# Performance work log

Measured on AMD Instinct MI355X. Metric: run time of the kernel, lower is better.

The kernel has to match this reference:

```python
import jax, jax.numpy as jnp
import numpy as np

N = 50000
NEG_SLOPE = 0.2  # PyG GATConv default negative_slope


def gat_conv(x, src, dst, W, a_src, a_dst, bias, concat):
    """One PyG-style GATConv (eval mode, self-loops already in src/dst).
    x: [N, F_in], W: [F_in, H*C], a_src/a_dst: [H, C], bias: [H*C] or [C].
    """
    H, C = a_src.shape
    xl = (x @ W).reshape(N, H, C)                      # [N, H, C]
    alpha_src = jnp.sum(xl * a_src, axis=-1)           # [N, H]
    alpha_dst = jnp.sum(xl * a_dst, axis=-1)           # [N, H]
    e = jax.nn.leaky_relu(alpha_src[src] + alpha_dst[dst], NEG_SLOPE)  # [E, H]
    # edge-softmax over incoming edges of each destination node
    m = jax.ops.segment_max(e, dst, num_segments=N)    # [N, H]
    e = jnp.exp(e - m[dst])
    s = jax.ops.segment_sum(e, dst, num_segments=N)    # [N, H]
    alpha = e / s[dst]                                 # [E, H]
    msg = xl[src] * alpha[:, :, None]                  # [E, H, C]
    out = jax.ops.segment_sum(msg, dst, num_segments=N)  # [N, H, C]
    out = out.reshape(N, H * C) if concat else out.mean(axis=1)
    return out + bias


def setup_inputs() -> dict:
    key = jax.random.key(0)
    ks = jax.random.split(key, 10)
    in_ch, hid, out_ch, heads = 128, 64, 64, 4
    E = 800000
    x = jax.random.normal(ks[0], (N, in_ch), dtype=jnp.float32)
    edge_index = jax.random.randint(ks[1], (2, E), 0, N, dtype=jnp.int64)
    s1 = 1.0 / np.sqrt(in_ch)
    s2 = 1.0 / np.sqrt(hid * heads)
    return {
        "x": x,
        "edge_index": edge_index,
        "W1": jax.random.normal(ks[2], (in_ch, heads * hid), jnp.float32) * s1,
        "att_src1": jax.random.normal(ks[3], (heads, hid), jnp.float32) * s1,
        "att_dst1": jax.random.normal(ks[4], (heads, hid), jnp.float32) * s1,
        "b1": jnp.zeros((heads * hid,), jnp.float32),
        "W2": jax.random.normal(ks[5], (heads * hid, out_ch), jnp.float32) * s2,
        "att_src2": jax.random.normal(ks[6], (1, out_ch), jnp.float32) * s2,
        "att_dst2": jax.random.normal(ks[7], (1, out_ch), jnp.float32) * s2,
        "b2": jnp.zeros((out_ch,), jnp.float32),
    }


def reference(x, edge_index, W1, att_src1, att_dst1, b1, W2, att_src2, att_dst2, b2):
    # PyG GATConv adds self-loops by default
    loops = jnp.arange(N, dtype=edge_index.dtype)
    src = jnp.concatenate([edge_index[0], loops])
    dst = jnp.concatenate([edge_index[1], loops])
    h = gat_conv(x, src, dst, W1, att_src1, att_dst1, b1, concat=True)
    h = jax.nn.elu(h)  # dropout is identity in eval mode
    out = gat_conv(h, src, dst, W2, att_src2, att_dst2, b2, concat=False)
    return out
```

## Files before the change

### kernel.cpp

```cpp
#include <hip/hip_runtime.h>
#include <math.h>


typedef unsigned short u16;
typedef short s8v __attribute__((ext_vector_type(8)));
typedef float f32x4 __attribute__((ext_vector_type(4)));

#define LOG2E 1.4426950408889634f

__device__ __forceinline__ float bflo(unsigned int u) {
  return __builtin_bit_cast(float, u << 16);
}
__device__ __forceinline__ float bfhi(unsigned int u) {
  return __builtin_bit_cast(float, u & 0xffff0000u);
}
__device__ __forceinline__ u16 f2bf(float f) {
  unsigned int u = __builtin_bit_cast(unsigned int, f);
  return (u16)((u + 0x7fff + ((u >> 16) & 1)) >> 16);
}


__global__ void prep_count_kernel(const int* __restrict__ ei, int E, int Nn,
                                  int* __restrict__ deg,
                                  const float* __restrict__ W1, u16* __restrict__ W1T,
                                  const float* __restrict__ W2, u16* __restrict__ W2T) {
  int i = blockIdx.x * blockDim.x + threadIdx.x;
  int Et = E + Nn;
  if (i < Et) {
    int dst = (i < E) ? ei[E + i] : (i - E);
    atomicAdd(&deg[dst], 1);
    return;
  }
  int e = i - Et;
  if (e < 128 * 256) {
    int k = e >> 8, n = e & 255;
    W1T[n * 128 + k] = f2bf(W1[e]);
    return;
  }
  e -= 128 * 256;
  if (e < 256 * 64) {
    int k = e >> 6, n = e & 63;
    W2T[n * 256 + k] = f2bf(W2[e]);
  }
}

__global__ void scan_partials_kernel(const int* __restrict__ deg,
                                     int* __restrict__ partials, int Ntot) {
  __shared__ int red[256];
  int t = threadIdx.x;
  int base = blockIdx.x * 1024 + t * 4;
  int s = 0;
  if (base + 3 < Ntot) {
    int4 v = *(const int4*)(deg + base);
    s = v.x + v.y + v.z + v.w;
  } else {
    for (int i = 0; i < 4; ++i)
      if (base + i < Ntot) s += deg[base + i];
  }
  red[t] = s;
  __syncthreads();
  for (int off = 128; off > 0; off >>= 1) {
    if (t < off) red[t] += red[t + off];
    __syncthreads();
  }
  if (t == 0) partials[blockIdx.x] = red[0];
}

__global__ void scan_final_kernel(const int* __restrict__ deg,
                                  const int* __restrict__ partials,
                                  int* __restrict__ rowptr,
                                  int* __restrict__ cursor, int Ntot, int NB) {
  __shared__ int sums[256];
  int t = threadIdx.x;
  int bid = blockIdx.x;
  int base = bid * 1024 + t * 4;
  int4 v = make_int4(0, 0, 0, 0);
  if (base + 3 < Ntot) {
    v = *(const int4*)(deg + base);
  } else {
    if (base + 0 < Ntot) v.x = deg[base + 0];
    if (base + 1 < Ntot) v.y = deg[base + 1];
    if (base + 2 < Ntot) v.z = deg[base + 2];
    if (base + 3 < Ntot) v.w = deg[base + 3];
  }
  sums[t] = v.x + v.y + v.z + v.w;
  __syncthreads();
  for (int off = 1; off < 256; off <<= 1) {
    int u = (t >= off) ? sums[t - off] : 0;
    __syncthreads();
    sums[t] += u;
    __syncthreads();
  }
  int boff = 0;
  for (int j = 0; j < bid; ++j) boff += partials[j];
  int excl = boff + ((t == 0) ? 0 : sums[t - 1]);
  int4 r;
  r.x = excl;
  r.y = r.x + v.x;
  r.z = r.y + v.y;
  r.w = r.z + v.z;
  if (base + 3 < Ntot) {
    *(int4*)(rowptr + base) = r;
    *(int4*)(cursor + base) = r;
  } else {
    if (base + 0 < Ntot) { rowptr[base + 0] = r.x; cursor[base + 0] = r.x; }
    if (base + 1 < Ntot) { rowptr[base + 1] = r.y; cursor[base + 1] = r.y; }
    if (base + 2 < Ntot) { rowptr[base + 2] = r.z; cursor[base + 2] = r.z; }
    if (base + 3 < Ntot) { rowptr[base + 3] = r.w; cursor[base + 3] = r.w; }
  }
}

__global__ void scatter_edges_kernel(const int* __restrict__ ei, int E, int Nn,
                                     int* __restrict__ cursor, int* __restrict__ col) {
  int e = blockIdx.x * blockDim.x + threadIdx.x;
  if (e >= E + Nn) return;
  int src, dst;
  if (e < E) { src = ei[e]; dst = ei[E + e]; }
  else       { src = dst = e - E; }
  int pos = atomicAdd(&cursor[dst], 1);
  col[pos] = src;
}


__global__ __launch_bounds__(256) void gemm1_fused_kernel(
    const float* __restrict__ x,
    const u16* __restrict__ w1t,
    const float* __restrict__ a_src,
    const float* __restrict__ a_dst,
    u16* __restrict__ C,
    float* __restrict__ asrc, float* __restrict__ adst,
    int M) {
  constexpr int PK = 136;
  __shared__ short As[128][PK];
  __shared__ short Bs[128][PK];
  int tid = threadIdx.x;
  int lane = tid & 63, w = tid >> 6;
  int q = lane >> 4, fr = lane & 15;
  int wm = (w >> 1) * 64, wn = (w & 1) * 64;
  int bm0 = blockIdx.x * 128;
  int fk = q * 8;

#pragma unroll
  for (int p = 0; p < 16; ++p) {
    int idx = p * 1024 + tid * 4;
    int r = idx >> 7, c = idx & 127;
    float4 v = make_float4(0.f, 0.f, 0.f, 0.f);
    if (bm0 + r < M) v = *(const float4*)(x + (size_t)(bm0 + r) * 128 + c);
    ushort4 o = make_ushort4(f2bf(v.x), f2bf(v.y), f2bf(v.z), f2bf(v.w));
    *(ushort4*)&As[r][c] = o;
  }
#pragma unroll
  for (int p = 0; p < 8; ++p) {
    int idx = p * 2048 + tid * 8;
    int r = idx >> 7, c = idx & 127;
    *(s8v*)&Bs[r][c] = *(const s8v*)(w1t + (size_t)r * 128 + c);
  }
  __syncthreads();

  for (int nh = 0; nh < 2; ++nh) {
    if (nh == 1) {
      __syncthreads();
#pragma unroll
      for (int p = 0; p < 8; ++p) {
        int idx = p * 2048 + tid * 8;
        int r = idx >> 7, c = idx & 127;
        *(s8v*)&Bs[r][c] = *(const s8v*)(w1t + (size_t)(128 + r) * 128 + c);
      }
      __syncthreads();
    }
    f32x4 acc[4][4] = {};
#pragma unroll
    for (int ks = 0; ks < 4; ++ks) {
      s8v af[4], bf[4];
#pragma unroll
      for (int i = 0; i < 4; ++i)
        af[i] = *(const s8v*)&As[wm + i * 16 + fr][ks * 32 + fk];
#pragma unroll
      for (int j = 0; j < 4; ++j)
        bf[j] = *(const s8v*)&Bs[wn + j * 16 + fr][ks * 32 + fk];
#pragma unroll
      for (int i = 0; i < 4; ++i)
#pragma unroll
        for (int j = 0; j < 4; ++j)
          acc[i][j] = __builtin_amdgcn_mfma_f32_16x16x32_bf16(af[i], bf[j], acc[i][j], 0, 0, 0);
    }

    int h = nh * 2 + (wn >> 6);
    float asv[4], adv[4];
#pragma unroll
    for (int j = 0; j < 4; ++j) {
      asv[j] = a_src[h * 64 + j * 16 + fr];
      adv[j] = a_dst[h * 64 + j * 16 + fr];
    }
#pragma unroll
    for (int i = 0; i < 4; ++i) {
#pragma unroll
      for (int r = 0; r < 4; ++r) {
        int row = bm0 + wm + i * 16 + q * 4 + r;
        float ps = 0.f, pd = 0.f;
#pragma unroll
        for (int j = 0; j < 4; ++j) {
          ps = fmaf(acc[i][j][r], asv[j], ps);
          pd = fmaf(acc[i][j][r], adv[j], pd);
        }
#pragma unroll
        for (int mmask = 1; mmask < 16; mmask <<= 1) {
          ps += __shfl_xor(ps, mmask, 64);
          pd += __shfl_xor(pd, mmask, 64);
        }
        if (fr == 0 && row < M) {
          asrc[row * 4 + h] = ps * LOG2E;
          adst[row * 4 + h] = pd * LOG2E;
        }
      }
    }
#pragma unroll
    for (int i = 0; i < 4; ++i)
#pragma unroll
      for (int j = 0; j < 4; ++j)
#pragma unroll
        for (int r = 0; r < 4; ++r) {
          int row = bm0 + wm + i * 16 + q * 4 + r;
          if (row < M)
            C[(size_t)row * 256 + nh * 128 + wn + j * 16 + fr] = f2bf(acc[i][j][r]);
        }
  }
}


__global__ __launch_bounds__(256) void gemm2_fused_kernel(
    const u16* __restrict__ A,
    const u16* __restrict__ Bt,
    const float* __restrict__ a_src,
    const float* __restrict__ a_dst,
    u16* __restrict__ C,
    float* __restrict__ asrc, float* __restrict__ adst,
    int M) {
  constexpr int BM = 128, BN = 64, BK = 32, PK = 40;
  __shared__ short As[BM][PK];
  __shared__ short Bs[BN][PK];
  __shared__ float alds[BM][4];
  int tid = threadIdx.x;
  int lane = tid & 63, w = tid >> 6;
  int q = lane >> 4, fr = lane & 15;
  int wm = (w >> 1) * 64, wn = (w & 1) * 32;
  int bm0 = blockIdx.x * BM;
  int fk = q * 8;

  f32x4 acc[4][2] = {};

  for (int k0 = 0; k0 < 256; k0 += BK) {
#pragma unroll
    for (int p = 0; p < 2; ++p) {
      int idx = p * 2048 + tid * 8;
      int r = idx / BK, c = idx % BK;
      *(s8v*)&As[r][c] = *(const s8v*)(A + (size_t)(bm0 + r) * 256 + k0 + c);
    }
    {
      int idx = tid * 8;
      int r = idx / BK, c = idx % BK;
      if (r < BN)
        *(s8v*)&Bs[r][c] = *(const s8v*)(Bt + (size_t)r * 256 + k0 + c);
    }
    __syncthreads();

    s8v af[4], bf[2];
#pragma unroll
    for (int i = 0; i < 4; ++i)
      af[i] = *(const s8v*)&As[wm + i * 16 + fr][fk];
#pragma unroll
    for (int j = 0; j < 2; ++j)
      bf[j] = *(const s8v*)&Bs[wn + j * 16 + fr][fk];
#pragma unroll
    for (int i = 0; i < 4; ++i)
#pragma unroll
      for (int j = 0; j < 2; ++j)
        acc[i][j] = __builtin_amdgcn_mfma_f32_16x16x32_bf16(af[i], bf[j], acc[i][j], 0, 0, 0);
    __syncthreads();
  }

  float asv[2], adv[2];
#pragma unroll
  for (int j = 0; j < 2; ++j) {
    asv[j] = a_src[wn + j * 16 + fr];
    adv[j] = a_dst[wn + j * 16 + fr];
  }
#pragma unroll
  for (int i = 0; i < 4; ++i) {
#pragma unroll
    for (int r = 0; r < 4; ++r) {
      int lr = wm + i * 16 + q * 4 + r;
      float ps = 0.f, pd = 0.f;
#pragma unroll
      for (int j = 0; j < 2; ++j) {
        ps = fmaf(acc[i][j][r], asv[j], ps);
        pd = fmaf(acc[i][j][r], adv[j], pd);
      }
#pragma unroll
      for (int mmask = 1; mmask < 16; mmask <<= 1) {
        ps += __shfl_xor(ps, mmask, 64);
        pd += __shfl_xor(pd, mmask, 64);
      }
      if (fr == 0) {
        alds[lr][(w & 1) * 2 + 0] = ps;
        alds[lr][(w & 1) * 2 + 1] = pd;
      }
    }
  }
#pragma unroll
  for (int i = 0; i < 4; ++i)
#pragma unroll
    for (int j = 0; j < 2; ++j)
#pragma unroll
      for (int r = 0; r < 4; ++r) {
        int row = bm0 + wm + i * 16 + q * 4 + r;
        if (row < M)
          C[(size_t)row * 64 + wn + j * 16 + fr] = f2bf(acc[i][j][r]);
      }
  __syncthreads();
  if (tid < BM) {
    int row = bm0 + tid;
    if (row < M) {
      asrc[row] = (alds[tid][0] + alds[tid][2]) * LOG2E;
      adst[row] = (alds[tid][1] + alds[tid][3]) * LOG2E;
    }
  }
}


__global__ void agg_multi_kernel(const u16* __restrict__ xlb,
                                 const float* __restrict__ asrc,
                                 const float* __restrict__ adst,
                                 const int* __restrict__ rowptr,
                                 const int* __restrict__ col,
                                 const float* __restrict__ bias,
                                 u16* __restrict__ hb, int Nn) {
  int n = blockIdx.x * 8 + (threadIdx.x >> 5);
  if (n >= Nn) return;
  int lane = threadIdx.x & 31;
  int h = lane >> 3;
  float adn = adst[n * 4 + h];
  int beg = rowptr[n], end = rowptr[n + 1];

  float s = 0.f;
  float acc[8] = {};

  float as0 = 0.f, as1 = 0.f, as2 = 0.f, as3 = 0.f;
  uint4 v0 = {}, v1 = {}, v2 = {}, v3 = {};
  {
    int sc = col[beg];
    as0 = asrc[sc * 4 + h];
    v0 = *(const uint4*)(xlb + (size_t)sc * 256 + lane * 8);
    if (beg + 1 < end) {
      int c1 = col[beg + 1];
      as1 = asrc[c1 * 4 + h];
      v1 = *(const uint4*)(xlb + (size_t)c1 * 256 + lane * 8);
    }
    if (beg + 2 < end) {
      int c2 = col[beg + 2];
      as2 = asrc[c2 * 4 + h];
      v2 = *(const uint4*)(xlb + (size_t)c2 * 256 + lane * 8);
    }
    if (beg + 3 < end) {
      int c3 = col[beg + 3];
      as3 = asrc[c3 * 4 + h];
      v3 = *(const uint4*)(xlb + (size_t)c3 * 256 + lane * 8);
    }
  }

  for (int i = beg; i < end; ++i) {
    float e = as0 + adn;
    e = fmaxf(e, 0.2f * e);
    uint4 vc = v0;
    as0 = as1; v0 = v1;
    as1 = as2; v1 = v2;
    as2 = as3; v2 = v3;
    if (i + 4 < end) {
      int sc = col[i + 4];
      as3 = asrc[sc * 4 + h];
      v3 = *(const uint4*)(xlb + (size_t)sc * 256 + lane * 8);
    }
    float w = __builtin_amdgcn_exp2f(e);
    s += w;
    acc[0] = fmaf(w, bflo(vc.x), acc[0]);
    acc[1] = fmaf(w, bfhi(vc.x), acc[1]);
    acc[2] = fmaf(w, bflo(vc.y), acc[2]);
    acc[3] = fmaf(w, bfhi(vc.y), acc[3]);
    acc[4] = fmaf(w, bflo(vc.z), acc[4]);
    acc[5] = fmaf(w, bfhi(vc.z), acc[5]);
    acc[6] = fmaf(w, bflo(vc.w), acc[6]);
    acc[7] = fmaf(w, bfhi(vc.w), acc[7]);
  }
  float inv_s = 1.f / s;

  float4 b0 = *(const float4*)(bias + lane * 8);
  float4 b1f = *(const float4*)(bias + lane * 8 + 4);
  float bb[8] = {b0.x, b0.y, b0.z, b0.w, b1f.x, b1f.y, b1f.z, b1f.w};
  u16 ov[8];
#pragma unroll
  for (int j = 0; j < 8; ++j) {
    float o = fmaf(acc[j], inv_s, bb[j]);
    o = (o > 0.f) ? o : __expf(o) - 1.f;
    ov[j] = f2bf(o);
  }
  *(uint4*)(hb + (size_t)n * 256 + lane * 8) = *(uint4*)ov;
}


__global__ void agg_single_kernel(const u16* __restrict__ xlb,
                                  const float* __restrict__ asrc,
                                  const float* __restrict__ adst,
                                  const int* __restrict__ rowptr,
                                  const int* __restrict__ col,
                                  const float* __restrict__ bias,
                                  float* __restrict__ out, int Nn) {
  int n = blockIdx.x * 32 + (threadIdx.x >> 3);
  if (n >= Nn) return;
  int lane = threadIdx.x & 7;
  float adn = adst[n];
  int beg = rowptr[n], end = rowptr[n + 1];

  float s = 0.f;
  float acc[8] = {};

  float as0 = 0.f, as1 = 0.f, as2 = 0.f;
  uint4 v0 = {}, v1 = {}, v2 = {};
  {
    int sc = col[beg];
    as0 = asrc[sc];
    v0 = *(const uint4*)(xlb + (size_t)sc * 64 + lane * 8);
    if (beg + 1 < end) {
      int c1 = col[beg + 1];
      as1 = asrc[c1];
      v1 = *(const uint4*)(xlb + (size_t)c1 * 64 + lane * 8);
    }
    if (beg + 2 < end) {
      int c2 = col[beg + 2];
      as2 = asrc[c2];
      v2 = *(const uint4*)(xlb + (size_t)c2 * 64 + lane * 8);
    }
  }

  for (int i = beg; i < end; ++i) {
    float e = as0 + adn;
    e = fmaxf(e, 0.2f * e);
    uint4 vc = v0;
    as0 = as1; v0 = v1;
    as1 = as2; v1 = v2;
    if (i + 3 < end) {
      int sc = col[i + 3];
      as2 = asrc[sc];
      v2 = *(const uint4*)(xlb + (size_t)sc * 64 + lane * 8);
    }
    float w = __builtin_amdgcn_exp2f(e);
    s += w;
    acc[0] = fmaf(w, bflo(vc.x), acc[0]);
    acc[1] = fmaf(w, bfhi(vc.x), acc[1]);
    acc[2] = fmaf(w, bflo(vc.y), acc[2]);
    acc[3] = fmaf(w, bfhi(vc.y), acc[3]);
    acc[4] = fmaf(w, bflo(vc.z), acc[4]);
    acc[5] = fmaf(w, bfhi(vc.z), acc[5]);
    acc[6] = fmaf(w, bflo(vc.w), acc[6]);
    acc[7] = fmaf(w, bfhi(vc.w), acc[7]);
  }
  float inv_s = 1.f / s;

  const float* bp = bias + lane * 8;
  float4 o0, o1;
  o0.x = fmaf(acc[0], inv_s, bp[0]);
  o0.y = fmaf(acc[1], inv_s, bp[1]);
  o0.z = fmaf(acc[2], inv_s, bp[2]);
  o0.w = fmaf(acc[3], inv_s, bp[3]);
  o1.x = fmaf(acc[4], inv_s, bp[4]);
  o1.y = fmaf(acc[5], inv_s, bp[5]);
  o1.z = fmaf(acc[6], inv_s, bp[6]);
  o1.w = fmaf(acc[7], inv_s, bp[7]);
  *(float4*)(out + (size_t)n * 64 + lane * 8) = o0;
  *(float4*)(out + (size_t)n * 64 + lane * 8 + 4) = o1;
}


extern "C" void kernel_launch(void* const* d_in, const int* in_sizes, int n_in,
                              void* d_out, int out_size, void* d_ws, size_t ws_size,
                              hipStream_t stream) {
  const float* x   = (const float*)d_in[0];
  const int*   ei  = (const int*)d_in[1];
  const float* W1  = (const float*)d_in[2];
  const float* as1 = (const float*)d_in[3];
  const float* ad1 = (const float*)d_in[4];
  const float* b1  = (const float*)d_in[5];
  const float* W2  = (const float*)d_in[6];
  const float* as2 = (const float*)d_in[7];
  const float* ad2 = (const float*)d_in[8];
  const float* b2  = (const float*)d_in[9];
  float* out = (float*)d_out;

  const int Nn = in_sizes[0] / 128;
  const int E  = in_sizes[1] / 2;
  const int Et = E + Nn;
  const int Ntot = Nn + 1;
  const int NB = (Ntot + 1023) / 1024;
  const int MB = (Nn + 127) / 128;
  const int Mpad = MB * 128;

  char* base = (char*)d_ws;
  size_t off = 0;
  auto alloc = [&](size_t bytes) -> void* {
    void* p = base + off;
    off = (off + bytes + 255) & ~(size_t)255;
    return p;
  };
  u16*   w1t      = (u16*)alloc((size_t)256 * 128 * 2);
  u16*   w2t      = (u16*)alloc((size_t)64 * 256 * 2);
  u16*   xlb1     = (u16*)alloc((size_t)Mpad * 256 * 2);
  u16*   hb       = (u16*)alloc((size_t)Mpad * 256 * 2);
  float* asrc1    = (float*)alloc((size_t)Nn * 4 * 4);
  float* adst1    = (float*)alloc((size_t)Nn * 4 * 4);
  float* asrc2    = (float*)alloc((size_t)Nn * 4);
  float* adst2    = (float*)alloc((size_t)Nn * 4);
  int*   deg      = (int*)alloc((size_t)(Ntot + 8) * 4);
  int*   rowptr   = (int*)alloc((size_t)(Ntot + 8) * 4);
  int*   cursor   = (int*)alloc((size_t)(Ntot + 8) * 4);
  int*   partials = (int*)alloc(256 * 4);
  int*   col      = (int*)alloc((size_t)Et * 4);
  u16*   xlb2     = xlb1;

  hipMemsetAsync(deg, 0, (size_t)Ntot * 4, stream);
  {
    int tot = Et + 128 * 256 + 256 * 64;
    prep_count_kernel<<<(tot + 255) / 256, 256, 0, stream>>>(
        ei, E, Nn, deg, W1, w1t, W2, w2t);
  }
  scan_partials_kernel<<<NB, 256, 0, stream>>>(deg, partials, Ntot);
  scan_final_kernel<<<NB, 256, 0, stream>>>(deg, partials, rowptr, cursor, Ntot, NB);
  scatter_edges_kernel<<<(Et + 255) / 256, 256, 0, stream>>>(ei, E, Nn, cursor, col);

  gemm1_fused_kernel<<<MB, 256, 0, stream>>>(x, w1t, as1, ad1, xlb1, asrc1, adst1, Nn);
  agg_multi_kernel<<<(Nn + 7) / 8, 256, 0, stream>>>(xlb1, asrc1, adst1, rowptr, col, b1, hb, Nn);

  gemm2_fused_kernel<<<MB, 256, 0, stream>>>(hb, w2t, as2, ad2, xlb2, asrc2, adst2, Nn);
  agg_single_kernel<<<(Nn + 31) / 32, 256, 0, stream>>>(xlb2, asrc2, adst2, rowptr, col, b2, out, Nn);
}
```

Measured before the change: 254.0 us.

## Merge CSR build into one cooperative kernel and split GEMM1 over N tiles

The memset, degree count, two scan kernels and edge scatter are replaced by a single cooperative kernel of 512 blocks that uses grid-wide syncs between phases, which removes several launches and their gaps. GEMM1 now uses a 2D grid with a K-loop over 32-wide tiles and smaller shared memory, so twice as many blocks run and occupancy rises, at the cost of reloading and re-converting the x tile for each N half. Grid-stride loops in the fused kernel may lower parallelism for the atomic phases, and the serial partials scan is done by a single thread.

```diff
diff --git a/kernel.cpp b/kernel.cpp
--- a/kernel.cpp
+++ b/kernel.cpp
@@ -1,5 +1,8 @@
 #include <hip/hip_runtime.h>
+#include <hip/hip_cooperative_groups.h>
 #include <math.h>
+
+namespace cg = cooperative_groups;
 
 
 typedef unsigned short u16;
@@ -20,105 +23,113 @@
 }
 
 
-__global__ void prep_count_kernel(const int* __restrict__ ei, int E, int Nn,
-                                  int* __restrict__ deg,
-                                  const float* __restrict__ W1, u16* __restrict__ W1T,
-                                  const float* __restrict__ W2, u16* __restrict__ W2T) {
-  int i = blockIdx.x * blockDim.x + threadIdx.x;
-  int Et = E + Nn;
-  if (i < Et) {
-    int dst = (i < E) ? ei[E + i] : (i - E);
-    atomicAdd(&deg[dst], 1);
-    return;
-  }
-  int e = i - Et;
-  if (e < 128 * 256) {
+__global__ __launch_bounds__(256) void csr_build_kernel(
+    const int* __restrict__ ei, int E, int Nn,
+    const float* __restrict__ W1, u16* __restrict__ W1T,
+    const float* __restrict__ W2, u16* __restrict__ W2T,
+    int* __restrict__ deg, int* __restrict__ rowptr,
+    int* __restrict__ cursor, int* __restrict__ col,
+    int* __restrict__ partials) {
+  cg::grid_group grid = cg::this_grid();
+  const int nthr = gridDim.x * blockDim.x;
+  const int gtid = blockIdx.x * blockDim.x + threadIdx.x;
+  const int t = threadIdx.x;
+  const int Ntot = Nn + 1;
+  const int Et = E + Nn;
+  const int NB = (Ntot + 1023) / 1024;
+  __shared__ int red[256];
+
+  for (int i = gtid; i < Ntot; i += nthr) deg[i] = 0;
+  for (int e = gtid; e < 128 * 256; e += nthr) {
     int k = e >> 8, n = e & 255;
     W1T[n * 128 + k] = f2bf(W1[e]);
-    return;
-  }
-  e -= 128 * 256;
-  if (e < 256 * 64) {
+  }
+  for (int e = gtid; e < 256 * 64; e += nthr) {
     int k = e >> 6, n = e & 63;
     W2T[n * 256 + k] = f2bf(W2[e]);
   }
-}
-
-__global__ void scan_partials_kernel(const int* __restrict__ deg,
-                                     int* __restrict__ partials, int Ntot) {
-  __shared__ int red[256];
-  int t = threadIdx.x;
-  int base = blockIdx.x * 1024 + t * 4;
-  int s = 0;
-  if (base + 3 < Ntot) {
-    int4 v = *(const int4*)(deg + base);
-    s = v.x + v.y + v.z + v.w;
-  } else {
-    for (int i = 0; i < 4; ++i)
-      if (base + i < Ntot) s += deg[base + i];
-  }
-  red[t] = s;
-  __syncthreads();
-  for (int off = 128; off > 0; off >>= 1) {
-    if (t < off) red[t] += red[t + off];
+  grid.sync();
+
+  for (int e = gtid; e < Et; e += nthr) {
+    int dst = (e < E) ? ei[E + e] : (e - E);
+    atomicAdd(&deg[dst], 1);
+  }
+  grid.sync();
+
+  if ((int)blockIdx.x < NB) {
+    int base = blockIdx.x * 1024 + t * 4;
+    int s = 0;
+    if (base + 3 < Ntot) {
+      int4 v = *(const int4*)(deg + base);
+      s = v.x + v.y + v.z + v.w;
+    } else {
+      for (int i = 0; i < 4; ++i)
+        if (base + i < Ntot) s += deg[base + i];
+    }
+    red[t] = s;
     __syncthreads();
-  }
-  if (t == 0) partials[blockIdx.x] = red[0];
-}
-
-__global__ void scan_final_kernel(const int* __restrict__ deg,
-                                  const int* __restrict__ partials,
-                                  int* __restrict__ rowptr,
-                                  int* __restrict__ cursor, int Ntot, int NB) {
-  __shared__ int sums[256];
-  int t = threadIdx.x;
-  int bid = blockIdx.x;
-  int base = bid * 1024 + t * 4;
-  int4 v = make_int4(0, 0, 0, 0);
-  if (base + 3 < Ntot) {
-    v = *(const int4*)(deg + base);
-  } else {
-    if (base + 0 < Ntot) v.x = deg[base + 0];
-    if (base + 1 < Ntot) v.y = deg[base + 1];
-    if (base + 2 < Ntot) v.z = deg[base + 2];
-    if (base + 3 < Ntot) v.w = deg[base + 3];
-  }
-  sums[t] = v.x + v.y + v.z + v.w;
-  __syncthreads();
-  for (int off = 1; off < 256; off <<= 1) {
-    int u = (t >= off) ? sums[t - off] : 0;
+    for (int off = 128; off > 0; off >>= 1) {
+      if (t < off) red[t] += red[t + off];
+      __syncthreads();
+    }
+    if (t == 0) partials[blockIdx.x] = red[0];
+  }
+  grid.sync();
+
+  if (blockIdx.x == 0 && t == 0) {
+    int run = 0;
+    for (int j = 0; j < NB; ++j) {
+      int v = partials[j];
+      partials[j] = run;
+      run += v;
+    }
+  }
+  grid.sync();
+
+  if ((int)blockIdx.x < NB) {
+    int base = blockIdx.x * 1024 + t * 4;
+    int4 v = make_int4(0, 0, 0, 0);
+    if (base + 3 < Ntot) {
+      v = *(const int4*)(deg + base);
+    } else {
+      if (base + 0 < Ntot) v.x = deg[base + 0];
+      if (base + 1 < Ntot) v.y = deg[base + 1];
+      if (base + 2 < Ntot) v.z = deg[base + 2];
+      if (base + 3 < Ntot) v.w = deg[base + 3];
+    }
+    red[t] = v.x + v.y + v.z + v.w;
     __syncthreads();
-    sums[t] += u;
-    __syncthreads();
-  }
-  int boff = 0;
-  for (int j = 0; j < bid; ++j) boff += partials[j];
-  int excl = boff + ((t == 0) ? 0 : sums[t - 1]);
-  int4 r;
-  r.x = excl;
-  r.y = r.x + v.x;
-  r.z = r.y + v.y;
-  r.w = r.z + v.z;
-  if (base + 3 < Ntot) {
-    *(int4*)(rowptr + base) = r;
-    *(int4*)(cursor + base) = r;
-  } else {
-    if (base + 0 < Ntot) { rowptr[base + 0] = r.x; cursor[base + 0] = r.x; }
-    if (base + 1 < Ntot) { rowptr[base + 1] = r.y; cursor[base + 1] = r.y; }
-    if (base + 2 < Ntot) { rowptr[base + 2] = r.z; cursor[base + 2] = r.z; }
-    if (base + 3 < Ntot) { rowptr[base + 3] = r.w; cursor[base + 3] = r.w; }
-  }
-}
-
-__global__ void scatter_edges_kernel(const int* __restrict__ ei, int E, int Nn,
-                                     int* __restrict__ cursor, int* __restrict__ col) {
-  int e = blockIdx.x * blockDim.x + threadIdx.x;
-  if (e >= E + Nn) return;
-  int src, dst;
-  if (e < E) { src = ei[e]; dst = ei[E + e]; }
-  else       { src = dst = e - E; }
-  int pos = atomicAdd(&cursor[dst], 1);
-  col[pos] = src;
+    for (int off = 1; off < 256; off <<= 1) {
+      int u = (t >= off) ? red[t - off] : 0;
+      __syncthreads();
+      red[t] += u;
+      __syncthreads();
+    }
+    int excl = partials[blockIdx.x] + ((t == 0) ? 0 : red[t - 1]);
+    int4 r;
+    r.x = excl;
+    r.y = r.x + v.x;
+    r.z = r.y + v.y;
+    r.w = r.z + v.z;
+    if (base + 3 < Ntot) {
+      *(int4*)(rowptr + base) = r;
+      *(int4*)(cursor + base) = r;
+    } else {
+      if (base + 0 < Ntot) { rowptr[base + 0] = r.x; cursor[base + 0] = r.x; }
+      if (base + 1 < Ntot) { rowptr[base + 1] = r.y; cursor[base + 1] = r.y; }
+      if (base + 2 < Ntot) { rowptr[base + 2] = r.z; cursor[base + 2] = r.z; }
+      if (base + 3 < Ntot) { rowptr[base + 3] = r.w; cursor[base + 3] = r.w; }
+    }
+  }
+  grid.sync();
+
+  for (int e = gtid; e < Et; e += nthr) {
+    int src, dst;
+    if (e < E) { src = ei[e]; dst = ei[E + e]; }
+    else       { src = dst = e - E; }
+    int pos = atomicAdd(&cursor[dst], 1);
+    col[pos] = src;
+  }
 }
 
 
@@ -130,101 +141,89 @@
     u16* __restrict__ C,
     float* __restrict__ asrc, float* __restrict__ adst,
     int M) {
-  constexpr int PK = 136;
-  __shared__ short As[128][PK];
-  __shared__ short Bs[128][PK];
+  constexpr int BM = 128, BN = 128, BK = 32, PK = 40;
+  __shared__ short As[BM][PK];
+  __shared__ short Bs[BN][PK];
   int tid = threadIdx.x;
   int lane = tid & 63, w = tid >> 6;
   int q = lane >> 4, fr = lane & 15;
   int wm = (w >> 1) * 64, wn = (w & 1) * 64;
-  int bm0 = blockIdx.x * 128;
+  int bm0 = blockIdx.x * BM, bn0 = blockIdx.y * BN;
   int fk = q * 8;
 
-#pragma unroll
-  for (int p = 0; p < 16; ++p) {
-    int idx = p * 1024 + tid * 4;
-    int r = idx >> 7, c = idx & 127;
-    float4 v = make_float4(0.f, 0.f, 0.f, 0.f);
-    if (bm0 + r < M) v = *(const float4*)(x + (size_t)(bm0 + r) * 128 + c);
-    ushort4 o = make_ushort4(f2bf(v.x), f2bf(v.y), f2bf(v.z), f2bf(v.w));
-    *(ushort4*)&As[r][c] = o;
-  }
-#pragma unroll
-  for (int p = 0; p < 8; ++p) {
-    int idx = p * 2048 + tid * 8;
-    int r = idx >> 7, c = idx & 127;
-    *(s8v*)&Bs[r][c] = *(const s8v*)(w1t + (size_t)r * 128 + c);
-  }
-  __syncthreads();
-
-  for (int nh = 0; nh < 2; ++nh) {
-    if (nh == 1) {
-      __syncthreads();
-#pragma unroll
-      for (int p = 0; p < 8; ++p) {
-        int idx = p * 2048 + tid * 8;
-        int r = idx >> 7, c = idx & 127;
-        *(s8v*)&Bs[r][c] = *(const s8v*)(w1t + (size_t)(128 + r) * 128 + c);
-      }
-      __syncthreads();
-    }
-    f32x4 acc[4][4] = {};
-#pragma unroll
-    for (int ks = 0; ks < 4; ++ks) {
-      s8v af[4], bf[4];
-#pragma unroll
-      for (int i = 0; i < 4; ++i)
-        af[i] = *(const s8v*)&As[wm + i * 16 + fr][ks * 32 + fk];
+  f32x4 acc[4][4] = {};
+
+  for (int k0 = 0; k0 < 128; k0 += BK) {
+#pragma unroll
+    for (int p = 0; p < 4; ++p) {
+      int idx = p * 1024 + tid * 4;
+      int r = idx >> 5, c = idx & 31;
+      float4 v = make_float4(0.f, 0.f, 0.f, 0.f);
+      if (bm0 + r < M) v = *(const float4*)(x + (size_t)(bm0 + r) * 128 + k0 + c);
+      *(ushort4*)&As[r][c] = make_ushort4(f2bf(v.x), f2bf(v.y), f2bf(v.z), f2bf(v.w));
+    }
+#pragma unroll
+    for (int p = 0; p < 2; ++p) {
+      int idx = p * 2048 + tid * 8;
+      int r = idx >> 5, c = idx & 31;
+      *(s8v*)&Bs[r][c] = *(const s8v*)(w1t + (size_t)(bn0 + r) * 128 + k0 + c);
+    }
+    __syncthreads();
+
+    s8v af[4], bf[4];
+#pragma unroll
+    for (int i = 0; i < 4; ++i)
+      af[i] = *(const s8v*)&As[wm + i * 16 + fr][fk];
+#pragma unroll
+    for (int j = 0; j < 4; ++j)
+      bf[j] = *(const s8v*)&Bs[wn + j * 16 + fr][fk];
+#pragma unroll
+    for (int i = 0; i < 4; ++i)
 #pragma unroll
       for (int j = 0; j < 4; ++j)
-        bf[j] = *(const s8v*)&Bs[wn + j * 16 + fr][ks * 32 + fk];
-#pragma unroll
-      for (int i = 0; i < 4; ++i)
-#pragma unroll
-        for (int j = 0; j < 4; ++j)
-          acc[i][j] = __builtin_amdgcn_mfma_f32_16x16x32_bf16(af[i], bf[j], acc[i][j], 0, 0, 0);
-    }
-
-    int h = nh * 2 + (wn >> 6);
-    float asv[4], adv[4];
-#pragma unroll
-    for (int j = 0; j < 4; ++j) {
-      asv[j] = a_src[h * 64 + j * 16 + fr];
-      adv[j] = a_dst[h * 64 + j * 16 + fr];
-    }
-#pragma unroll
-    for (int i = 0; i < 4; ++i) {
+        acc[i][j] = __builtin_amdgcn_mfma_f32_16x16x32_bf16(af[i], bf[j], acc[i][j], 0, 0, 0);
+    __syncthreads();
+  }
+
+  int h = blockIdx.y * 2 + (wn >> 6);
+  float asv[4], adv[4];
+#pragma unroll
+  for (int j = 0; j < 4; ++j) {
+    asv[j] = a_src[h * 64 + j * 16 + fr];
+    adv[j] = a_dst[h * 64 + j * 16 + fr];
+  }
+#pragma unroll
+  for (int i = 0; i < 4; ++i) {
+#pragma unroll
+    for (int r = 0; r < 4; ++r) {
+      int row = bm0 + wm + i * 16 + q * 4 + r;
+      float ps = 0.f, pd = 0.f;
+#pragma unroll
+      for (int j = 0; j < 4; ++j) {
+        ps = fmaf(acc[i][j][r], asv[j], ps);
+        pd = fmaf(acc[i][j][r], adv[j], pd);
+      }
+#pragma unroll
+      for (int mmask = 1; mmask < 16; mmask <<= 1) {
+        ps += __shfl_xor(ps, mmask, 64);
+        pd += __shfl_xor(pd, mmask, 64);
+      }
+      if (fr == 0 && row < M) {
+        asrc[row * 4 + h] = ps * LOG2E;
+        adst[row * 4 + h] = pd * LOG2E;
+      }
+    }
+  }
+#pragma unroll
+  for (int i = 0; i < 4; ++i)
+#pragma unroll
+    for (int j = 0; j < 4; ++j)
 #pragma unroll
       for (int r = 0; r < 4; ++r) {
         int row = bm0 + wm + i * 16 + q * 4 + r;
-        float ps = 0.f, pd = 0.f;
-#pragma unroll
-        for (int j = 0; j < 4; ++j) {
-          ps = fmaf(acc[i][j][r], asv[j], ps);
-          pd = fmaf(acc[i][j][r], adv[j], pd);
-        }
-#pragma unroll
-        for (int mmask = 1; mmask < 16; mmask <<= 1) {
-          ps += __shfl_xor(ps, mmask, 64);
-          pd += __shfl_xor(pd, mmask, 64);
-        }
-        if (fr == 0 && row < M) {
-          asrc[row * 4 + h] = ps * LOG2E;
-          adst[row * 4 + h] = pd * LOG2E;
-        }
-      }
-    }
-#pragma unroll
-    for (int i = 0; i < 4; ++i)
-#pragma unroll
-      for (int j = 0; j < 4; ++j)
-#pragma unroll
-        for (int r = 0; r < 4; ++r) {
-          int row = bm0 + wm + i * 16 + q * 4 + r;
-          if (row < M)
-            C[(size_t)row * 256 + nh * 128 + wn + j * 16 + fr] = f2bf(acc[i][j][r]);
-        }
-  }
+        if (row < M)
+          C[(size_t)row * 256 + bn0 + wn + j * 16 + fr] = f2bf(acc[i][j][r]);
+      }
 }
 
 
@@ -499,7 +498,6 @@
   const int E  = in_sizes[1] / 2;
   const int Et = E + Nn;
   const int Ntot = Nn + 1;
-  const int NB = (Ntot + 1023) / 1024;
   const int MB = (Nn + 127) / 128;
   const int Mpad = MB * 128;
 
@@ -525,17 +523,24 @@
   int*   col      = (int*)alloc((size_t)Et * 4);
   u16*   xlb2     = xlb1;
 
-  hipMemsetAsync(deg, 0, (size_t)Ntot * 4, stream);
   {
-    int tot = Et + 128 * 256 + 256 * 64;
-    prep_count_kernel<<<(tot + 255) / 256, 256, 0, stream>>>(
-        ei, E, Nn, deg, W1, w1t, W2, w2t);
-  }
-  scan_partials_kernel<<<NB, 256, 0, stream>>>(deg, partials, Ntot);
-  scan_final_kernel<<<NB, 256, 0, stream>>>(deg, partials, rowptr, cursor, Ntot, NB);
-  scatter_edges_kernel<<<(Et + 255) / 256, 256, 0, stream>>>(ei, E, Nn, cursor, col);
-
-  gemm1_fused_kernel<<<MB, 256, 0, stream>>>(x, w1t, as1, ad1, xlb1, asrc1, adst1, Nn);
+    const int* ei_ = ei; int E_ = E, Nn_ = Nn;
+    const float* W1_ = W1; u16* w1t_ = w1t;
+    const float* W2_ = W2; u16* w2t_ = w2t;
+    int* deg_ = deg; int* rowptr_ = rowptr; int* cursor_ = cursor;
+    int* col_ = col; int* partials_ = partials;
+    void* args[] = {(void*)&ei_, (void*)&E_, (void*)&Nn_,
+                    (void*)&W1_, (void*)&w1t_, (void*)&W2_, (void*)&w2t_,
+                    (void*)&deg_, (void*)&rowptr_, (void*)&cursor_,
+                    (void*)&col_, (void*)&partials_};
+    hipLaunchCooperativeKernel((void*)csr_build_kernel, dim3(512), dim3(256),
+                               args, 0, stream);
+  }
+
+  {
+    dim3 grid(MB, 2);
+    gemm1_fused_kernel<<<grid, 256, 0, stream>>>(x, w1t, as1, ad1, xlb1, asrc1, adst1, Nn);
+  }
   agg_multi_kernel<<<(Nn + 7) / 8, 256, 0, stream>>>(xlb1, asrc1, adst1, rowptr, col, b1, hb, Nn);
 
   gemm2_fused_kernel<<<MB, 256, 0, stream>>>(hb, w2t, as2, ad2, xlb2, asrc2, adst2, Nn);
```

Measured after the change: 522.1 us. 2.06x slower.

## Split gemm1 over two column blocks with K-tiled shared memory

Applied to the files above, without the earlier changes.

Rewrites the first GEMM so each block computes one 128-column half over a 2D grid, loading K in slices of 32 instead of staging the full 128-wide A and B tiles in shared memory. This cuts LDS use per block from about 68KB to about 20KB, which should raise occupancy, and doubles the number of blocks. The cost is that x is read and converted to bf16 twice (once per column block), and there are more barriers per K step with no prefetch overlap.

```diff
diff --git a/kernel.cpp b/kernel.cpp
--- a/kernel.cpp
+++ b/kernel.cpp
@@ -130,101 +130,89 @@
     u16* __restrict__ C,
     float* __restrict__ asrc, float* __restrict__ adst,
     int M) {
-  constexpr int PK = 136;
-  __shared__ short As[128][PK];
-  __shared__ short Bs[128][PK];
+  constexpr int BM = 128, BN = 128, BK = 32, PK = 40;
+  __shared__ short As[BM][PK];
+  __shared__ short Bs[BN][PK];
   int tid = threadIdx.x;
   int lane = tid & 63, w = tid >> 6;
   int q = lane >> 4, fr = lane & 15;
   int wm = (w >> 1) * 64, wn = (w & 1) * 64;
-  int bm0 = blockIdx.x * 128;
+  int bm0 = blockIdx.x * BM, bn0 = blockIdx.y * BN;
   int fk = q * 8;
 
-#pragma unroll
-  for (int p = 0; p < 16; ++p) {
-    int idx = p * 1024 + tid * 4;
-    int r = idx >> 7, c = idx & 127;
-    float4 v = make_float4(0.f, 0.f, 0.f, 0.f);
-    if (bm0 + r < M) v = *(const float4*)(x + (size_t)(bm0 + r) * 128 + c);
-    ushort4 o = make_ushort4(f2bf(v.x), f2bf(v.y), f2bf(v.z), f2bf(v.w));
-    *(ushort4*)&As[r][c] = o;
-  }
-#pragma unroll
-  for (int p = 0; p < 8; ++p) {
-    int idx = p * 2048 + tid * 8;
-    int r = idx >> 7, c = idx & 127;
-    *(s8v*)&Bs[r][c] = *(const s8v*)(w1t + (size_t)r * 128 + c);
-  }
-  __syncthreads();
-
-  for (int nh = 0; nh < 2; ++nh) {
-    if (nh == 1) {
-      __syncthreads();
-#pragma unroll
-      for (int p = 0; p < 8; ++p) {
-        int idx = p * 2048 + tid * 8;
-        int r = idx >> 7, c = idx & 127;
-        *(s8v*)&Bs[r][c] = *(const s8v*)(w1t + (size_t)(128 + r) * 128 + c);
-      }
-      __syncthreads();
-    }
-    f32x4 acc[4][4] = {};
-#pragma unroll
-    for (int ks = 0; ks < 4; ++ks) {
-      s8v af[4], bf[4];
-#pragma unroll
-      for (int i = 0; i < 4; ++i)
-        af[i] = *(const s8v*)&As[wm + i * 16 + fr][ks * 32 + fk];
+  f32x4 acc[4][4] = {};
+
+  for (int k0 = 0; k0 < 128; k0 += BK) {
+#pragma unroll
+    for (int p = 0; p < 4; ++p) {
+      int idx = p * 1024 + tid * 4;
+      int r = idx >> 5, c = idx & 31;
+      float4 v = make_float4(0.f, 0.f, 0.f, 0.f);
+      if (bm0 + r < M) v = *(const float4*)(x + (size_t)(bm0 + r) * 128 + k0 + c);
+      *(ushort4*)&As[r][c] = make_ushort4(f2bf(v.x), f2bf(v.y), f2bf(v.z), f2bf(v.w));
+    }
+#pragma unroll
+    for (int p = 0; p < 2; ++p) {
+      int idx = p * 2048 + tid * 8;
+      int r = idx >> 5, c = idx & 31;
+      *(s8v*)&Bs[r][c] = *(const s8v*)(w1t + (size_t)(bn0 + r) * 128 + k0 + c);
+    }
+    __syncthreads();
+
+    s8v af[4], bf[4];
+#pragma unroll
+    for (int i = 0; i < 4; ++i)
+      af[i] = *(const s8v*)&As[wm + i * 16 + fr][fk];
+#pragma unroll
+    for (int j = 0; j < 4; ++j)
+      bf[j] = *(const s8v*)&Bs[wn + j * 16 + fr][fk];
+#pragma unroll
+    for (int i = 0; i < 4; ++i)
 #pragma unroll
       for (int j = 0; j < 4; ++j)
-        bf[j] = *(const s8v*)&Bs[wn + j * 16 + fr][ks * 32 + fk];
-#pragma unroll
-      for (int i = 0; i < 4; ++i)
-#pragma unroll
-        for (int j = 0; j < 4; ++j)
-          acc[i][j] = __builtin_amdgcn_mfma_f32_16x16x32_bf16(af[i], bf[j], acc[i][j], 0, 0, 0);
-    }
-
-    int h = nh * 2 + (wn >> 6);
-    float asv[4], adv[4];
-#pragma unroll
-    for (int j = 0; j < 4; ++j) {
-      asv[j] = a_src[h * 64 + j * 16 + fr];
-      adv[j] = a_dst[h * 64 + j * 16 + fr];
-    }
-#pragma unroll
-    for (int i = 0; i < 4; ++i) {
+        acc[i][j] = __builtin_amdgcn_mfma_f32_16x16x32_bf16(af[i], bf[j], acc[i][j], 0, 0, 0);
+    __syncthreads();
+  }
+
+  int h = blockIdx.y * 2 + (wn >> 6);
+  float asv[4], adv[4];
+#pragma unroll
+  for (int j = 0; j < 4; ++j) {
+    asv[j] = a_src[h * 64 + j * 16 + fr];
+    adv[j] = a_dst[h * 64 + j * 16 + fr];
+  }
+#pragma unroll
+  for (int i = 0; i < 4; ++i) {
+#pragma unroll
+    for (int r = 0; r < 4; ++r) {
+      int row = bm0 + wm + i * 16 + q * 4 + r;
+      float ps = 0.f, pd = 0.f;
+#pragma unroll
+      for (int j = 0; j < 4; ++j) {
+        ps = fmaf(acc[i][j][r], asv[j], ps);
+        pd = fmaf(acc[i][j][r], adv[j], pd);
+      }
+#pragma unroll
+      for (int mmask = 1; mmask < 16; mmask <<= 1) {
+        ps += __shfl_xor(ps, mmask, 64);
+        pd += __shfl_xor(pd, mmask, 64);
+      }
+      if (fr == 0 && row < M) {
+        asrc[row * 4 + h] = ps * LOG2E;
+        adst[row * 4 + h] = pd * LOG2E;
+      }
+    }
+  }
+#pragma unroll
+  for (int i = 0; i < 4; ++i)
+#pragma unroll
+    for (int j = 0; j < 4; ++j)
 #pragma unroll
       for (int r = 0; r < 4; ++r) {
         int row = bm0 + wm + i * 16 + q * 4 + r;
-        float ps = 0.f, pd = 0.f;
-#pragma unroll
-        for (int j = 0; j < 4; ++j) {
-          ps = fmaf(acc[i][j][r], asv[j], ps);
-          pd = fmaf(acc[i][j][r], adv[j], pd);
-        }
-#pragma unroll
-        for (int mmask = 1; mmask < 16; mmask <<= 1) {
-          ps += __shfl_xor(ps, mmask, 64);
-          pd += __shfl_xor(pd, mmask, 64);
-        }
-        if (fr == 0 && row < M) {
-          asrc[row * 4 + h] = ps * LOG2E;
-          adst[row * 4 + h] = pd * LOG2E;
-        }
-      }
-    }
-#pragma unroll
-    for (int i = 0; i < 4; ++i)
-#pragma unroll
-      for (int j = 0; j < 4; ++j)
-#pragma unroll
-        for (int r = 0; r < 4; ++r) {
-          int row = bm0 + wm + i * 16 + q * 4 + r;
-          if (row < M)
-            C[(size_t)row * 256 + nh * 128 + wn + j * 16 + fr] = f2bf(acc[i][j][r]);
-        }
-  }
+        if (row < M)
+          C[(size_t)row * 256 + bn0 + wn + j * 16 + fr] = f2bf(acc[i][j][r]);
+      }
 }
 
 
@@ -535,7 +523,10 @@
   scan_final_kernel<<<NB, 256, 0, stream>>>(deg, partials, rowptr, cursor, Ntot, NB);
   scatter_edges_kernel<<<(Et + 255) / 256, 256, 0, stream>>>(ei, E, Nn, cursor, col);
 
-  gemm1_fused_kernel<<<MB, 256, 0, stream>>>(x, w1t, as1, ad1, xlb1, asrc1, adst1, Nn);
+  {
+    dim3 grid(MB, 2);
+    gemm1_fused_kernel<<<grid, 256, 0, stream>>>(x, w1t, as1, ad1, xlb1, asrc1, adst1, Nn);
+  }
   agg_multi_kernel<<<(Nn + 7) / 8, 256, 0, stream>>>(xlb1, asrc1, adst1, rowptr, col, b1, hb, Nn);
 
   gemm2_fused_kernel<<<MB, 256, 0, stream>>>(hb, w2t, as2, ad2, xlb2, asrc2, adst2, Nn);
```

Result: faster. 245.5 us (median of 2 runs) (-3.3%).
